# Optimization experiments

Hardware: AMD Instinct MI355X
Metric: run time of the kernel (lower is better)

## Reference

```python
import jax, jax.numpy as jnp
import numpy as np

N, B, C, H = 2048, 2, 1024, 16
HD = C // H


def setup_inputs() -> dict:
    key = jax.random.key(0)
    ks = jax.random.split(key, 11)
    s = 0.02
    return {
        "query": jax.random.normal(ks[0], (N, B, C), jnp.float32),
        "key": jax.random.normal(ks[1], (N, B, C), jnp.float32),
        "value": jax.random.normal(ks[2], (B, N, C), jnp.float32),
        "num_heads": H,
        "Wq": jax.random.normal(ks[3], (C, C), jnp.float32) * s,
        "bq": jnp.zeros((C,), jnp.float32),
        "Wk": jax.random.normal(ks[4], (C, HD), jnp.float32) * s,
        "bk": jnp.zeros((HD,), jnp.float32),
        "Wv": jax.random.normal(ks[5], (C, HD), jnp.float32) * s,
        "bv": jnp.zeros((HD,), jnp.float32),
        "Wp": jax.random.normal(ks[6], (C, C), jnp.float32) * s,
        "bp": jnp.zeros((C,), jnp.float32),
    }


def reference(query, key, value, num_heads, Wq, bq, Wk, bk, Wv, bv, Wp, bp):
    # query/key arrive seq-first (N,B,C); permute to batch-first as in torch code
    k_in = jnp.transpose(key, (1, 0, 2))    # (B, Nk, C)
    q_in = jnp.transpose(query, (1, 0, 2))  # (B, Nq, C)
    Bsz, Nq, Cd = q_in.shape
    hd = Cd // num_heads
    scale = hd ** -0.5

    # shared single K/V head (MQA)
    k = k_in @ Wk + bk                      # (B, Nk, hd)
    v = value @ Wv + bv                     # (B, Nk, hd)
    q = (q_in @ Wq + bq).reshape(Bsz, Nq, num_heads, hd)
    q = jnp.transpose(q, (0, 2, 1, 3)) * scale  # (B, H, Nq, hd)

    attn = jnp.einsum('bhqd,bkd->bhqk', q, k)   # (B, H, Nq, Nk)
    attn = jax.nn.softmax(attn, axis=-1)
    x = jnp.einsum('bhqk,bkd->bhqd', attn, v)   # (B, H, Nq, hd)
    x = jnp.transpose(x, (0, 2, 1, 3)).reshape(Bsz, Nq, Cd)
    x = x @ Wp + bp
    return jnp.transpose(x, (1, 0, 2))          # (Nq, B, C)
```

## Files before the change

### kernel.cpp

```cpp
#include <hip/hip_runtime.h>
#include <hip/hip_bf16.h>

#define DI __device__ __forceinline__

typedef float f32x4 __attribute__((ext_vector_type(4)));
typedef float f32x16 __attribute__((ext_vector_type(16)));
typedef short s16x8 __attribute__((ext_vector_type(8)));
typedef unsigned short u16x4 __attribute__((ext_vector_type(4)));
typedef unsigned long long u64;


DI unsigned short f2bf(float x) {
  union { float f; unsigned u; } v; v.f = x;
  unsigned r = 0x7fffu + ((v.u >> 16) & 1u);
  return (unsigned short)((v.u + r) >> 16);
}

DI unsigned cvtpk(float lo, float hi) {
  unsigned u;
  asm("v_cvt_pk_bf16_f32 %0, %1, %2" : "=v"(u) : "v"(lo), "v"(hi));
  return u;
}

DI f32x16 zero16() {
  f32x16 z;
#pragma unroll
  for (int i = 0; i < 16; ++i) z[i] = 0.f;
  return z;
}

DI float max16(const f32x16& a) {
  float m0 = fmaxf(a[0], a[1]),  m1 = fmaxf(a[2], a[3]);
  float m2 = fmaxf(a[4], a[5]),  m3 = fmaxf(a[6], a[7]);
  float m4 = fmaxf(a[8], a[9]),  m5 = fmaxf(a[10], a[11]);
  float m6 = fmaxf(a[12], a[13]), m7 = fmaxf(a[14], a[15]);
  m0 = fmaxf(m0, m1); m2 = fmaxf(m2, m3); m4 = fmaxf(m4, m5); m6 = fmaxf(m6, m7);
  return fmaxf(fmaxf(m0, m2), fmaxf(m4, m6));
}

DI float sum16(const f32x16& a) {
  float s0 = a[0] + a[1],  s1 = a[2] + a[3];
  float s2 = a[4] + a[5],  s3 = a[6] + a[7];
  float s4 = a[8] + a[9],  s5 = a[10] + a[11];
  float s6 = a[12] + a[13], s7 = a[14] + a[15];
  s0 += s1; s2 += s3; s4 += s5; s6 += s7;
  return (s0 + s2) + (s4 + s6);
}

DI void gll16(const void* g, void* l) {
  __builtin_amdgcn_global_load_lds(
      (const __attribute__((address_space(1))) void*)g,
      (__attribute__((address_space(3))) void*)l, 16, 0, 0);
}

DI f32x16 mfma32(s16x8 a, s16x8 b, f32x16 c) {
  return __builtin_amdgcn_mfma_f32_32x32x16_bf16(a, b, c, 0, 0, 0);
}

DI f32x4 mfma16(s16x8 a, s16x8 b, f32x4 c) {
  return __builtin_amdgcn_mfma_f32_16x16x32_bf16(a, b, c, 0, 0, 0);
}

__global__ __launch_bounds__(256) void wconv_kernel(
    const float* __restrict__ Wq, const float* __restrict__ Wk,
    const float* __restrict__ Wv, const float* __restrict__ Wp,
    unsigned short* __restrict__ WqT, unsigned short* __restrict__ WkT,
    unsigned short* __restrict__ WvT, unsigned short* __restrict__ WpT)
{
  int bid = blockIdx.x;
  const float* W; unsigned short* WT; int Ncols; int base;
  if (bid < 512)       { W = Wq; WT = WqT; Ncols = 1024; base = bid; }
  else if (bid < 1024) { W = Wp; WT = WpT; Ncols = 1024; base = bid - 512; }
  else if (bid < 1056) { W = Wk; WT = WkT; Ncols = 64;   base = bid - 1024; }
  else                 { W = Wv; WT = WvT; Ncols = 64;   base = bid - 1056; }
  int nb = base >> 5, kb = base & 31;
  int n = nb * 64 + (threadIdx.x & 63);
  int k = kb * 32 + (threadIdx.x >> 6) * 8;
  float f[8];
#pragma unroll
  for (int i = 0; i < 8; ++i) f[i] = W[(size_t)(k + i) * Ncols + n];
  union { unsigned u[4]; s16x8 v; } x;
#pragma unroll
  for (int i = 0; i < 4; ++i) x.u[i] = cvtpk(f[2 * i], f[2 * i + 1]);
  *(s16x8*)(WT + (size_t)n * 1024 + k) = x.v;
}

__global__ __launch_bounds__(256) void cvt1_kernel(
    const float* __restrict__ q, unsigned short* __restrict__ qbf)
{
  int gid = blockIdx.x * 256 + threadIdx.x;
  int row = gid >> 7;
  int c8 = (gid & 127) << 3;
  int b = row >> 11, n = row & 2047;
  size_t soff = ((size_t)n * 2 + b) * 1024 + c8;
  f32x4 v0 = *(const f32x4*)(q + soff);
  f32x4 v1 = *(const f32x4*)(q + soff + 4);
  union { unsigned u[4]; s16x8 v; } x;
  x.u[0] = cvtpk(v0.x, v0.y); x.u[1] = cvtpk(v0.z, v0.w);
  x.u[2] = cvtpk(v1.x, v1.y); x.u[3] = cvtpk(v1.z, v1.w);
  *(s16x8*)(qbf + (size_t)row * 1024 + c8) = x.v;
}

template<int MODE>
__global__ __launch_bounds__(256) void gemm16_kernel(
    const unsigned short* __restrict__ A, const unsigned short* __restrict__ Bt,
    const float* __restrict__ bias, void* __restrict__ Cpv, float scale)
{
  __shared__ __align__(16) unsigned short Asub[2][128 * 64];
  __shared__ __align__(16) unsigned short Bsub[2][64 * 64];

  const int tid = threadIdx.x;
  const int lane = tid & 63, wave = tid >> 6;
  const int l16 = lane & 15, kq = lane >> 4;
  const int wr = wave >> 1, wc = wave & 1;
  const int row0 = blockIdx.x * 128;
  const int col0 = blockIdx.y * 64;

  f32x4 acc[4][2];
#pragma unroll
  for (int mi = 0; mi < 4; ++mi)
#pragma unroll
    for (int nj = 0; nj < 2; ++nj) acc[mi][nj] = f32x4{0.f, 0.f, 0.f, 0.f};

  auto STAGE = [&](int bf, int kt) {
    const int k0 = kt * 64;
#pragma unroll
    for (int i = 0; i < 4; ++i) {
      int o = i * 4096 + tid * 16;
      int r = o >> 7, c = (o & 127) >> 1;
      gll16(A + (size_t)(row0 + r) * 1024 + k0 + c,
            (char*)Asub[bf] + i * 4096 + wave * 1024);
    }
#pragma unroll
    for (int i = 0; i < 2; ++i) {
      int o = i * 4096 + tid * 16;
      int r = o >> 7, c = (o & 127) >> 1;
      gll16(Bt + (size_t)(col0 + r) * 1024 + k0 + c,
            (char*)Bsub[bf] + i * 4096 + wave * 1024);
    }
  };

  STAGE(0, 0);
  __syncthreads();
  int cur = 0;
  for (int kt = 0; kt < 16; ++kt) {
    if (kt + 1 < 16) STAGE(cur ^ 1, kt + 1);
#pragma unroll
    for (int ks = 0; ks < 2; ++ks) {
      s16x8 af[4]; s16x8 bf2[2];
#pragma unroll
      for (int mi = 0; mi < 4; ++mi)
        af[mi] = *(const s16x8*)(Asub[cur] + (wr * 64 + mi * 16 + l16) * 64 + ks * 32 + kq * 8);
#pragma unroll
      for (int nj = 0; nj < 2; ++nj)
        bf2[nj] = *(const s16x8*)(Bsub[cur] + (wc * 32 + nj * 16 + l16) * 64 + ks * 32 + kq * 8);
#pragma unroll
      for (int mi = 0; mi < 4; ++mi)
#pragma unroll
        for (int nj = 0; nj < 2; ++nj)
          acc[mi][nj] = mfma16(af[mi], bf2[nj], acc[mi][nj]);
    }
    __syncthreads();
    cur ^= 1;
  }

#pragma unroll
  for (int mi = 0; mi < 4; ++mi)
#pragma unroll
  for (int nj = 0; nj < 2; ++nj) {
    int col = col0 + wc * 32 + nj * 16 + l16;
    int rowb = row0 + wr * 64 + mi * 16 + kq * 4;
    float bv = bias[col];
#pragma unroll
    for (int r = 0; r < 4; ++r) {
      int row = rowb + r;
      float val = acc[mi][nj][r] + bv;
      if constexpr (MODE == 0) {
        ((unsigned short*)Cpv)[(size_t)row * 1024 + col] = f2bf(val * scale);
      } else {
        ((float*)Cpv)[(size_t)(row & 2047) * 2048 + (size_t)(row >> 11) * 1024 + col] = val;
      }
    }
  }
}

__global__ __launch_bounds__(256) void gemmkv_kernel(
    const float* __restrict__ Akey, const float* __restrict__ Aval,
    const unsigned short* __restrict__ Wk, const unsigned short* __restrict__ Wv,
    float* __restrict__ part)
{
  __shared__ __align__(16) unsigned short Asub[2][64 * 64];
  __shared__ __align__(16) unsigned short Bsub[2][64 * 64];

  const int tid = threadIdx.x;
  const int lane = tid & 63, wave = tid >> 6;
  const int l16 = lane & 15, kq = lane >> 4;
  const int wr = wave >> 1, wc = wave & 1;
  const int sel = blockIdx.y;
  const float* Af = sel ? Aval : Akey;
  const unsigned short* Bt = sel ? Wv : Wk;
  const int row0 = blockIdx.x * 64;
  const int kt0 = blockIdx.z * 4, kt1 = kt0 + 4;

  const int ar = tid >> 2, ac = (tid & 3) * 16;
  const int gm = row0 + ar;
  const size_t grow = sel ? (size_t)gm * 1024
                          : (size_t)((gm & 2047) * 2 + (gm >> 11)) * 1024;

  auto LOADA = [&](int kt, f32x4* a4) {
#pragma unroll
    for (int i = 0; i < 4; ++i)
      a4[i] = *(const f32x4*)(Af + grow + kt * 64 + ac + i * 4);
  };
  auto WRITEA = [&](int bf, const f32x4* a4) {
    union { unsigned u[8]; s16x8 v[2]; } x;
#pragma unroll
    for (int i = 0; i < 4; ++i) {
      x.u[2 * i]     = cvtpk(a4[i].x, a4[i].y);
      x.u[2 * i + 1] = cvtpk(a4[i].z, a4[i].w);
    }
    *(s16x8*)(Asub[bf] + ar * 64 + ac)     = x.v[0];
    *(s16x8*)(Asub[bf] + ar * 64 + ac + 8) = x.v[1];
  };
  auto STAGEB = [&](int bf, int kt) {
#pragma unroll
    for (int i = 0; i < 2; ++i) {
      int o = i * 4096 + tid * 16;
      int r = o >> 7, c = (o & 127) >> 1;
      gll16(Bt + (size_t)r * 1024 + kt * 64 + c,
            (char*)Bsub[bf] + i * 4096 + wave * 1024);
    }
  };

  f32x4 acc[2][2];
#pragma unroll
  for (int mi = 0; mi < 2; ++mi)
#pragma unroll
    for (int nj = 0; nj < 2; ++nj) acc[mi][nj] = f32x4{0.f, 0.f, 0.f, 0.f};

  f32x4 a4[4];
  LOADA(kt0, a4);
  STAGEB(0, kt0);
  WRITEA(0, a4);
  __syncthreads();
  int cur = 0;
  for (int kt = kt0; kt < kt1; ++kt) {
    if (kt + 1 < kt1) { LOADA(kt + 1, a4); STAGEB(cur ^ 1, kt + 1); }
#pragma unroll
    for (int ks = 0; ks < 2; ++ks) {
      s16x8 af[2]; s16x8 bf2[2];
#pragma unroll
      for (int mi = 0; mi < 2; ++mi)
        af[mi] = *(const s16x8*)(Asub[cur] + (wr * 32 + mi * 16 + l16) * 64 + ks * 32 + kq * 8);
#pragma unroll
      for (int nj = 0; nj < 2; ++nj)
        bf2[nj] = *(const s16x8*)(Bsub[cur] + (wc * 32 + nj * 16 + l16) * 64 + ks * 32 + kq * 8);
#pragma unroll
      for (int mi = 0; mi < 2; ++mi)
#pragma unroll
        for (int nj = 0; nj < 2; ++nj)
          acc[mi][nj] = mfma16(af[mi], bf2[nj], acc[mi][nj]);
    }
    if (kt + 1 < kt1) WRITEA(cur ^ 1, a4);
    __syncthreads();
    cur ^= 1;
  }

#pragma unroll
  for (int mi = 0; mi < 2; ++mi)
#pragma unroll
  for (int nj = 0; nj < 2; ++nj) {
    int col = wc * 32 + nj * 16 + l16;
    int rowb = row0 + wr * 32 + mi * 16 + kq * 4;
#pragma unroll
    for (int r = 0; r < 4; ++r)
      part[(((size_t)blockIdx.z * 2 + sel) * 4096 + rowb + r) * 64 + col] = acc[mi][nj][r];
  }
}

__global__ __launch_bounds__(256) void kvreduce_kernel(
    const float* __restrict__ part, const float* __restrict__ bk,
    const float* __restrict__ bv, unsigned short* __restrict__ kproj,
    unsigned short* __restrict__ vprojT)
{
  int gid = blockIdx.x * 256 + threadIdx.x;
  int kv = gid >> 18;
  int rem = gid & 262143;
  int row = rem >> 6, col = rem & 63;
  float s = 0.f;
#pragma unroll
  for (int z = 0; z < 4; ++z)
    s += part[(((size_t)z * 2 + kv) * 4096 + row) * 64 + col];
  s += (kv ? bv : bk)[col];
  if (kv == 0)
    kproj[(size_t)row * 64 + col] = f2bf(s);
  else
    vprojT[(size_t)(row >> 11) * 131072 + (size_t)col * 2048 + (row & 2047)] = f2bf(s);
}

__global__ __launch_bounds__(512, 4) void attn_kernel(
    const unsigned short* __restrict__ qp, const unsigned short* __restrict__ kp,
    const unsigned short* __restrict__ vpt, unsigned short* __restrict__ xout)
{
  constexpr int KSTR = 72;
  __shared__ unsigned short SM[36864];
#define KBUF(c, hh) (SM + ((c) * 2 + (hh)) * (64 * KSTR))
#define VBUF(c, hh) (SM + 18432 + ((c) * 2 + (hh)) * (64 * KSTR))

  const int tid = threadIdx.x;
  const int lane = tid & 63, wave = tid >> 6;
  const int lq = lane & 31, hi = lane >> 5;
  const int qsub = wave & 3, half = wave >> 2;
  const int b = blockIdx.y >> 4, h = blockIdx.y & 15;
  const int q0 = blockIdx.x * 128 + qsub * 32;
  const size_t qrow = (size_t)(b * 2048 + q0 + lq);

  s16x8 qf[4];
#pragma unroll
  for (int s = 0; s < 4; ++s)
    qf[s] = *(const s16x8*)(qp + qrow * 1024 + h * 64 + s * 16 + hi * 8);

  f32x16 xacc0 = zero16(), xacc1 = zero16();
  float mrun = -1e30f, ssum = 0.f;

  const unsigned short* kb = kp + (size_t)b * (2048 * 64);
  const unsigned short* vb = vpt + (size_t)b * (64 * 2048);

  const int srow = tid >> 3;
  const int scol = (tid & 7) * 8;

  s16x8 kA, kB, vA, vB;
  {
    kA = *(const s16x8*)(kb + (size_t)srow * 64 + scol);
    kB = *(const s16x8*)(kb + (size_t)(16 * 64 + srow) * 64 + scol);
    vA = *(const s16x8*)(vb + (size_t)srow * 2048 + scol);
    vB = *(const s16x8*)(vb + (size_t)srow * 2048 + 16 * 64 + scol);
    *(s16x8*)(KBUF(0, 0) + srow * KSTR + scol) = kA;
    *(s16x8*)(KBUF(0, 1) + srow * KSTR + scol) = kB;
    *(s16x8*)(VBUF(0, 0) + srow * KSTR + scol) = vA;
    *(s16x8*)(VBUF(0, 1) + srow * KSTR + scol) = vB;
  }
  int cur = 0;

  for (int it = 0; it < 16; ++it) {
    __syncthreads();
    if (it + 1 < 16) {
      kA = *(const s16x8*)(kb + (size_t)((it + 1) * 64 + srow) * 64 + scol);
      kB = *(const s16x8*)(kb + (size_t)((it + 17) * 64 + srow) * 64 + scol);
      vA = *(const s16x8*)(vb + (size_t)srow * 2048 + (it + 1) * 64 + scol);
      vB = *(const s16x8*)(vb + (size_t)srow * 2048 + (it + 17) * 64 + scol);
    }
    const unsigned short* Kc = KBUF(cur, half);
    const unsigned short* Vc = VBUF(cur, half);

    f32x16 sacc0 = zero16(), sacc1 = zero16();
    __builtin_amdgcn_s_setprio(1);
#pragma unroll
    for (int s = 0; s < 4; ++s) {
      int c = s * 16 + hi * 8;
      s16x8 kf0 = *(const s16x8*)(Kc + lq * KSTR + c);
      s16x8 kf1 = *(const s16x8*)(Kc + (32 + lq) * KSTR + c);
      sacc0 = mfma32(kf0, qf[s], sacc0);
      sacc1 = mfma32(kf1, qf[s], sacc1);
    }
    __builtin_amdgcn_s_setprio(0);

    float tm = fmaxf(max16(sacc0), max16(sacc1));
    tm = fmaxf(tm, __shfl_xor(tm, 32));
    if (!__all(tm <= mrun + 8.f)) {
      float mnew = fmaxf(mrun, tm);
      float alpha = __builtin_amdgcn_exp2f(mrun - mnew);
      ssum *= alpha;
#pragma unroll
      for (int e = 0; e < 16; ++e) { xacc0[e] *= alpha; xacc1[e] *= alpha; }
      mrun = mnew;
    }
    f32x16 p0, p1;
#pragma unroll
    for (int e = 0; e < 16; ++e) p0[e] = __builtin_amdgcn_exp2f(sacc0[e] - mrun);
#pragma unroll
    for (int e = 0; e < 16; ++e) p1[e] = __builtin_amdgcn_exp2f(sacc1[e] - mrun);
    float tsum = sum16(p0) + sum16(p1);
    tsum += __shfl_xor(tsum, 32);
    ssum += tsum;

    s16x8 pb[4];
#pragma unroll
    for (int grp = 0; grp < 4; ++grp) {
      const f32x16& pp = (grp < 2) ? p0 : p1;
      const int eb = (grp & 1) * 8;
      unsigned A  = cvtpk(pp[eb + 0], pp[eb + 1]);
      unsigned Bw = cvtpk(pp[eb + 2], pp[eb + 3]);
      unsigned Cw = cvtpk(pp[eb + 4], pp[eb + 5]);
      unsigned Dw = cvtpk(pp[eb + 6], pp[eb + 7]);
      unsigned rA = (unsigned)__shfl_xor((int)(hi ? A : Cw), 32);
      unsigned rB = (unsigned)__shfl_xor((int)(hi ? Bw : Dw), 32);
      union { unsigned u[4]; s16x8 v; } pk_;
      pk_.u[0] = hi ? rA : A;
      pk_.u[1] = hi ? rB : Bw;
      pk_.u[2] = hi ? Cw : rA;
      pk_.u[3] = hi ? Dw : rB;
      pb[grp] = pk_.v;
    }

    __builtin_amdgcn_s_setprio(1);
#pragma unroll
    for (int kvs = 0; kvs < 4; ++kvs) {
      int c = kvs * 16 + hi * 8;
      s16x8 vf0 = *(const s16x8*)(Vc + lq * KSTR + c);
      s16x8 vf1 = *(const s16x8*)(Vc + (32 + lq) * KSTR + c);
      xacc0 = mfma32(vf0, pb[kvs], xacc0);
      xacc1 = mfma32(vf1, pb[kvs], xacc1);
    }
    __builtin_amdgcn_s_setprio(0);

    if (it + 1 < 16) {
      *(s16x8*)(KBUF(cur ^ 1, 0) + srow * KSTR + scol) = kA;
      *(s16x8*)(KBUF(cur ^ 1, 1) + srow * KSTR + scol) = kB;
      *(s16x8*)(VBUF(cur ^ 1, 0) + srow * KSTR + scol) = vA;
      *(s16x8*)(VBUF(cur ^ 1, 1) + srow * KSTR + scol) = vB;
      cur ^= 1;
    }
  }

  __syncthreads();
  float* msc = (float*)SM;
  const int mi_ = (qsub * 64 + lane) * 37;
  if (half == 1) {
#pragma unroll
    for (int e = 0; e < 16; ++e) { msc[mi_ + e] = xacc0[e]; msc[mi_ + 16 + e] = xacc1[e]; }
    msc[mi_ + 32] = mrun;
    msc[mi_ + 33] = ssum;
  }
  __syncthreads();
  if (half == 0) {
    float pm = msc[mi_ + 32], ps = msc[mi_ + 33];
    float mf = fmaxf(mrun, pm);
    float aa = __builtin_amdgcn_exp2f(mrun - mf);
    float bb = __builtin_amdgcn_exp2f(pm - mf);
    float inv = 1.0f / (ssum * aa + ps * bb);
#pragma unroll
    for (int dj = 0; dj < 2; ++dj) {
      const f32x16 xa = dj ? xacc1 : xacc0;
#pragma unroll
      for (int g = 0; g < 4; ++g) {
        u16x4 o4;
#pragma unroll
        for (int r = 0; r < 4; ++r) {
          int e = g * 4 + r;
          float merged = xa[e] * aa + msc[mi_ + dj * 16 + e] * bb;
          o4[r] = f2bf(merged * inv);
        }
        int d0 = dj * 32 + 8 * g + 4 * hi;
        *(u16x4*)(xout + qrow * 1024 + h * 64 + d0) = o4;
      }
    }
  }
#undef KBUF
#undef VBUF
}

extern "C" void kernel_launch(void* const* d_in, const int* in_sizes, int n_in,
                              void* d_out, int out_size, void* d_ws, size_t ws_size,
                              hipStream_t stream)
{
  const float* query = (const float*)d_in[0];
  const float* key   = (const float*)d_in[1];
  const float* value = (const float*)d_in[2];
  const float* Wq = (const float*)d_in[4];
  const float* bq = (const float*)d_in[5];
  const float* Wk = (const float*)d_in[6];
  const float* bk = (const float*)d_in[7];
  const float* Wv = (const float*)d_in[8];
  const float* bv = (const float*)d_in[9];
  const float* Wp = (const float*)d_in[10];
  const float* bp = (const float*)d_in[11];

  char* ws = (char*)d_ws;
  unsigned short* WqT    = (unsigned short*)(ws);
  unsigned short* WpT    = (unsigned short*)(ws + (2u << 20));
  unsigned short* WkT    = (unsigned short*)(ws + (4u << 20));
  unsigned short* WvT    = (unsigned short*)(ws + (4u << 20) + (128u << 10));
  unsigned short* kproj  = (unsigned short*)(ws + (5u << 20));
  unsigned short* vprojT = (unsigned short*)(ws + (5u << 20) + (512u << 10));
  unsigned short* qproj  = (unsigned short*)(ws + (6u << 20));
  unsigned short* xbuf   = (unsigned short*)(ws + (15u << 20));
  float*          part   = (float*)xbuf;
  unsigned short* qbf    = (unsigned short*)d_out;

  wconv_kernel<<<dim3(1088), 256, 0, stream>>>(Wq, Wk, Wv, Wp, WqT, WkT, WvT, WpT);
  cvt1_kernel<<<dim3(2048), 256, 0, stream>>>(query, qbf);

  const float qscale = 0.18033688011112042f;
  gemm16_kernel<0><<<dim3(32, 16), 256, 0, stream>>>(qbf, WqT, bq, qproj, qscale);
  gemmkv_kernel<<<dim3(64, 2, 4), 256, 0, stream>>>(key, value, WkT, WvT, part);
  kvreduce_kernel<<<dim3(2048), 256, 0, stream>>>(part, bk, bv, kproj, vprojT);
  attn_kernel<<<dim3(16, 32), 512, 0, stream>>>(qproj, kproj, vprojT, xbuf);
  gemm16_kernel<2><<<dim3(32, 16), 256, 0, stream>>>(xbuf, WpT, bp, d_out, 1.0f);
}
```

Baseline: 121.9 us.

## Fuse prep and projection GEMM launches, compute softmax rowsum via MFMA

Merges the weight-transpose and query-convert kernels into one prep launch, and runs the Q projection GEMM and the K/V projection GEMM in one launch using shared LDS. In attention, the softmax row sum is accumulated with an extra MFMA against a ones vector instead of VALU reductions and a shuffle, and the row max uses v_max3. The aim is to cut launch overhead and tail idle time and to shift VALU work onto the matrix cores. The cost is extra MFMA work per tile and a larger LDS footprint for the KV blocks.

```diff
diff --git a/kernel.cpp b/kernel.cpp
--- a/kernel.cpp
+++ b/kernel.cpp
@@ -22,6 +22,12 @@
   return u;
 }
 
+DI float max3f(float a, float b, float c) {
+  float d;
+  asm("v_max3_f32 %0, %1, %2, %3" : "=v"(d) : "v"(a), "v"(b), "v"(c));
+  return d;
+}
+
 DI f32x16 zero16() {
   f32x16 z;
 #pragma unroll
@@ -29,22 +35,15 @@
   return z;
 }
 
-DI float max16(const f32x16& a) {
-  float m0 = fmaxf(a[0], a[1]),  m1 = fmaxf(a[2], a[3]);
-  float m2 = fmaxf(a[4], a[5]),  m3 = fmaxf(a[6], a[7]);
-  float m4 = fmaxf(a[8], a[9]),  m5 = fmaxf(a[10], a[11]);
-  float m6 = fmaxf(a[12], a[13]), m7 = fmaxf(a[14], a[15]);
-  m0 = fmaxf(m0, m1); m2 = fmaxf(m2, m3); m4 = fmaxf(m4, m5); m6 = fmaxf(m6, m7);
-  return fmaxf(fmaxf(m0, m2), fmaxf(m4, m6));
-}
-
-DI float sum16(const f32x16& a) {
-  float s0 = a[0] + a[1],  s1 = a[2] + a[3];
-  float s2 = a[4] + a[5],  s3 = a[6] + a[7];
-  float s4 = a[8] + a[9],  s5 = a[10] + a[11];
-  float s6 = a[12] + a[13], s7 = a[14] + a[15];
-  s0 += s1; s2 += s3; s4 += s5; s6 += s7;
-  return (s0 + s2) + (s4 + s6);
+DI float max16_3(const f32x16& a) {
+  float m0 = max3f(a[0], a[1], a[2]);
+  float m1 = max3f(a[3], a[4], a[5]);
+  float m2 = max3f(a[6], a[7], a[8]);
+  float m3 = max3f(a[9], a[10], a[11]);
+  float m4 = max3f(a[12], a[13], a[14]);
+  float n0 = max3f(m0, m1, m2);
+  float n1 = max3f(m3, m4, a[15]);
+  return fmaxf(n0, n1);
 }
 
 DI void gll16(const void* g, void* l) {
@@ -61,18 +60,34 @@
   return __builtin_amdgcn_mfma_f32_16x16x32_bf16(a, b, c, 0, 0, 0);
 }
 
-__global__ __launch_bounds__(256) void wconv_kernel(
+__global__ __launch_bounds__(256) void prep_kernel(
+    const float* __restrict__ q, unsigned short* __restrict__ qbf,
     const float* __restrict__ Wq, const float* __restrict__ Wk,
     const float* __restrict__ Wv, const float* __restrict__ Wp,
     unsigned short* __restrict__ WqT, unsigned short* __restrict__ WkT,
     unsigned short* __restrict__ WvT, unsigned short* __restrict__ WpT)
 {
   int bid = blockIdx.x;
+  if (bid < 2048) {
+    int gid = bid * 256 + threadIdx.x;
+    int row = gid >> 7;
+    int c8 = (gid & 127) << 3;
+    int b = row >> 11, n = row & 2047;
+    size_t soff = ((size_t)n * 2 + b) * 1024 + c8;
+    f32x4 v0 = *(const f32x4*)(q + soff);
+    f32x4 v1 = *(const f32x4*)(q + soff + 4);
+    union { unsigned u[4]; s16x8 v; } x;
+    x.u[0] = cvtpk(v0.x, v0.y); x.u[1] = cvtpk(v0.z, v0.w);
+    x.u[2] = cvtpk(v1.x, v1.y); x.u[3] = cvtpk(v1.z, v1.w);
+    *(s16x8*)(qbf + (size_t)row * 1024 + c8) = x.v;
+    return;
+  }
+  int wb = bid - 2048;
   const float* W; unsigned short* WT; int Ncols; int base;
-  if (bid < 512)       { W = Wq; WT = WqT; Ncols = 1024; base = bid; }
-  else if (bid < 1024) { W = Wp; WT = WpT; Ncols = 1024; base = bid - 512; }
-  else if (bid < 1056) { W = Wk; WT = WkT; Ncols = 64;   base = bid - 1024; }
-  else                 { W = Wv; WT = WvT; Ncols = 64;   base = bid - 1056; }
+  if (wb < 512)       { W = Wq; WT = WqT; Ncols = 1024; base = wb; }
+  else if (wb < 1024) { W = Wp; WT = WpT; Ncols = 1024; base = wb - 512; }
+  else if (wb < 1056) { W = Wk; WT = WkT; Ncols = 64;   base = wb - 1024; }
+  else                { W = Wv; WT = WvT; Ncols = 64;   base = wb - 1056; }
   int nb = base >> 5, kb = base & 31;
   int n = nb * 64 + (threadIdx.x & 63);
   int k = kb * 32 + (threadIdx.x >> 6) * 8;
@@ -85,36 +100,19 @@
   *(s16x8*)(WT + (size_t)n * 1024 + k) = x.v;
 }
 
-__global__ __launch_bounds__(256) void cvt1_kernel(
-    const float* __restrict__ q, unsigned short* __restrict__ qbf)
-{
-  int gid = blockIdx.x * 256 + threadIdx.x;
-  int row = gid >> 7;
-  int c8 = (gid & 127) << 3;
-  int b = row >> 11, n = row & 2047;
-  size_t soff = ((size_t)n * 2 + b) * 1024 + c8;
-  f32x4 v0 = *(const f32x4*)(q + soff);
-  f32x4 v1 = *(const f32x4*)(q + soff + 4);
-  union { unsigned u[4]; s16x8 v; } x;
-  x.u[0] = cvtpk(v0.x, v0.y); x.u[1] = cvtpk(v0.z, v0.w);
-  x.u[2] = cvtpk(v1.x, v1.y); x.u[3] = cvtpk(v1.z, v1.w);
-  *(s16x8*)(qbf + (size_t)row * 1024 + c8) = x.v;
-}
-
 template<int MODE>
-__global__ __launch_bounds__(256) void gemm16_kernel(
-    const unsigned short* __restrict__ A, const unsigned short* __restrict__ Bt,
-    const float* __restrict__ bias, void* __restrict__ Cpv, float scale)
-{
-  __shared__ __align__(16) unsigned short Asub[2][128 * 64];
-  __shared__ __align__(16) unsigned short Bsub[2][64 * 64];
-
+DI void gemm16_body(const unsigned short* __restrict__ A,
+                    const unsigned short* __restrict__ Bt,
+                    const float* __restrict__ bias, void* __restrict__ Cpv,
+                    float scale, int bx, int by,
+                    unsigned short* As, unsigned short* Bs)
+{
   const int tid = threadIdx.x;
   const int lane = tid & 63, wave = tid >> 6;
   const int l16 = lane & 15, kq = lane >> 4;
   const int wr = wave >> 1, wc = wave & 1;
-  const int row0 = blockIdx.x * 128;
-  const int col0 = blockIdx.y * 64;
+  const int row0 = bx * 128;
+  const int col0 = by * 64;
 
   f32x4 acc[4][2];
 #pragma unroll
@@ -124,19 +122,19 @@
 
   auto STAGE = [&](int bf, int kt) {
     const int k0 = kt * 64;
+    char* Ad = (char*)As + bf * 16384;
+    char* Bd = (char*)Bs + bf * 8192;
 #pragma unroll
     for (int i = 0; i < 4; ++i) {
       int o = i * 4096 + tid * 16;
       int r = o >> 7, c = (o & 127) >> 1;
-      gll16(A + (size_t)(row0 + r) * 1024 + k0 + c,
-            (char*)Asub[bf] + i * 4096 + wave * 1024);
+      gll16(A + (size_t)(row0 + r) * 1024 + k0 + c, Ad + i * 4096 + wave * 1024);
     }
 #pragma unroll
     for (int i = 0; i < 2; ++i) {
       int o = i * 4096 + tid * 16;
       int r = o >> 7, c = (o & 127) >> 1;
-      gll16(Bt + (size_t)(col0 + r) * 1024 + k0 + c,
-            (char*)Bsub[bf] + i * 4096 + wave * 1024);
+      gll16(Bt + (size_t)(col0 + r) * 1024 + k0 + c, Bd + i * 4096 + wave * 1024);
     }
   };
 
@@ -150,10 +148,10 @@
       s16x8 af[4]; s16x8 bf2[2];
 #pragma unroll
       for (int mi = 0; mi < 4; ++mi)
-        af[mi] = *(const s16x8*)(Asub[cur] + (wr * 64 + mi * 16 + l16) * 64 + ks * 32 + kq * 8);
+        af[mi] = *(const s16x8*)(As + cur * 8192 + (wr * 64 + mi * 16 + l16) * 64 + ks * 32 + kq * 8);
 #pragma unroll
       for (int nj = 0; nj < 2; ++nj)
-        bf2[nj] = *(const s16x8*)(Bsub[cur] + (wc * 32 + nj * 16 + l16) * 64 + ks * 32 + kq * 8);
+        bf2[nj] = *(const s16x8*)(Bs + cur * 4096 + (wc * 32 + nj * 16 + l16) * 64 + ks * 32 + kq * 8);
 #pragma unroll
       for (int mi = 0; mi < 4; ++mi)
 #pragma unroll
@@ -184,23 +182,20 @@
   }
 }
 
-__global__ __launch_bounds__(256) void gemmkv_kernel(
-    const float* __restrict__ Akey, const float* __restrict__ Aval,
-    const unsigned short* __restrict__ Wk, const unsigned short* __restrict__ Wv,
-    float* __restrict__ part)
-{
-  __shared__ __align__(16) unsigned short Asub[2][64 * 64];
-  __shared__ __align__(16) unsigned short Bsub[2][64 * 64];
-
+DI void gemmkv_body(const float* __restrict__ Akey, const float* __restrict__ Aval,
+                    const unsigned short* __restrict__ Wk,
+                    const unsigned short* __restrict__ Wv,
+                    float* __restrict__ part, int bx, int sel, int bz,
+                    unsigned short* As, unsigned short* Bs)
+{
   const int tid = threadIdx.x;
   const int lane = tid & 63, wave = tid >> 6;
   const int l16 = lane & 15, kq = lane >> 4;
   const int wr = wave >> 1, wc = wave & 1;
-  const int sel = blockIdx.y;
   const float* Af = sel ? Aval : Akey;
   const unsigned short* Bt = sel ? Wv : Wk;
-  const int row0 = blockIdx.x * 64;
-  const int kt0 = blockIdx.z * 4, kt1 = kt0 + 4;
+  const int row0 = bx * 64;
+  const int kt0 = bz * 4, kt1 = kt0 + 4;
 
   const int ar = tid >> 2, ac = (tid & 3) * 16;
   const int gm = row0 + ar;
@@ -219,8 +214,8 @@
       x.u[2 * i]     = cvtpk(a4[i].x, a4[i].y);
       x.u[2 * i + 1] = cvtpk(a4[i].z, a4[i].w);
     }
-    *(s16x8*)(Asub[bf] + ar * 64 + ac)     = x.v[0];
-    *(s16x8*)(Asub[bf] + ar * 64 + ac + 8) = x.v[1];
+    *(s16x8*)(As + bf * 4096 + ar * 64 + ac)     = x.v[0];
+    *(s16x8*)(As + bf * 4096 + ar * 64 + ac + 8) = x.v[1];
   };
   auto STAGEB = [&](int bf, int kt) {
 #pragma unroll
@@ -228,7 +223,7 @@
       int o = i * 4096 + tid * 16;
       int r = o >> 7, c = (o & 127) >> 1;
       gll16(Bt + (size_t)r * 1024 + kt * 64 + c,
-            (char*)Bsub[bf] + i * 4096 + wave * 1024);
+            (char*)Bs + bf * 8192 + i * 4096 + wave * 1024);
     }
   };
 
@@ -251,10 +246,10 @@
       s16x8 af[2]; s16x8 bf2[2];
 #pragma unroll
       for (int mi = 0; mi < 2; ++mi)
-        af[mi] = *(const s16x8*)(Asub[cur] + (wr * 32 + mi * 16 + l16) * 64 + ks * 32 + kq * 8);
+        af[mi] = *(const s16x8*)(As + cur * 4096 + (wr * 32 + mi * 16 + l16) * 64 + ks * 32 + kq * 8);
 #pragma unroll
       for (int nj = 0; nj < 2; ++nj)
-        bf2[nj] = *(const s16x8*)(Bsub[cur] + (wc * 32 + nj * 16 + l16) * 64 + ks * 32 + kq * 8);
+        bf2[nj] = *(const s16x8*)(Bs + cur * 4096 + (wc * 32 + nj * 16 + l16) * 64 + ks * 32 + kq * 8);
 #pragma unroll
       for (int mi = 0; mi < 2; ++mi)
 #pragma unroll
@@ -274,8 +269,36 @@
     int rowb = row0 + wr * 32 + mi * 16 + kq * 4;
 #pragma unroll
     for (int r = 0; r < 4; ++r)
-      part[(((size_t)blockIdx.z * 2 + sel) * 4096 + rowb + r) * 64 + col] = acc[mi][nj][r];
-  }
+      part[(((size_t)bz * 2 + sel) * 4096 + rowb + r) * 64 + col] = acc[mi][nj][r];
+  }
+}
+
+__global__ __launch_bounds__(256) void gemmqkv_kernel(
+    const unsigned short* __restrict__ qbf, const unsigned short* __restrict__ WqT,
+    const float* __restrict__ bq, unsigned short* __restrict__ qproj, float qscale,
+    const float* __restrict__ key, const float* __restrict__ value,
+    const unsigned short* __restrict__ WkT, const unsigned short* __restrict__ WvT,
+    float* __restrict__ part)
+{
+  __shared__ __align__(16) unsigned short SMEM[24576];
+  int bid = blockIdx.x;
+  if (bid < 512) {
+    gemm16_body<0>(qbf, WqT, bq, qproj, qscale, bid & 31, bid >> 5,
+                   SMEM, SMEM + 16384);
+  } else {
+    int idx = bid - 512;
+    gemmkv_body(key, value, WkT, WvT, part, idx & 63, (idx >> 6) & 1, idx >> 7,
+                SMEM, SMEM + 8192);
+  }
+}
+
+__global__ __launch_bounds__(256) void gemmout_kernel(
+    const unsigned short* __restrict__ A, const unsigned short* __restrict__ Bt,
+    const float* __restrict__ bias, float* __restrict__ Cpv)
+{
+  __shared__ __align__(16) unsigned short SMEM[24576];
+  gemm16_body<2>(A, Bt, bias, (void*)Cpv, 1.0f, blockIdx.x, blockIdx.y,
+                 SMEM, SMEM + 16384);
 }
 
 __global__ __launch_bounds__(256) void kvreduce_kernel(
@@ -320,8 +343,12 @@
   for (int s = 0; s < 4; ++s)
     qf[s] = *(const s16x8*)(qp + qrow * 1024 + h * 64 + s * 16 + hi * 8);
 
-  f32x16 xacc0 = zero16(), xacc1 = zero16();
-  float mrun = -1e30f, ssum = 0.f;
+  s16x8 ones8;
+#pragma unroll
+  for (int i = 0; i < 8; ++i) ones8[i] = (short)0x3F80;
+
+  f32x16 xacc0 = zero16(), xacc1 = zero16(), xsum = zero16();
+  float mrun = -1e30f;
 
   const unsigned short* kb = kp + (size_t)b * (2048 * 64);
   const unsigned short* vb = vpt + (size_t)b * (64 * 2048);
@@ -365,12 +392,12 @@
     }
     __builtin_amdgcn_s_setprio(0);
 
-    float tm = fmaxf(max16(sacc0), max16(sacc1));
+    float tm = fmaxf(max16_3(sacc0), max16_3(sacc1));
     tm = fmaxf(tm, __shfl_xor(tm, 32));
     if (!__all(tm <= mrun + 8.f)) {
       float mnew = fmaxf(mrun, tm);
       float alpha = __builtin_amdgcn_exp2f(mrun - mnew);
-      ssum *= alpha;
+      xsum[0] *= alpha;
 #pragma unroll
       for (int e = 0; e < 16; ++e) { xacc0[e] *= alpha; xacc1[e] *= alpha; }
       mrun = mnew;
@@ -380,9 +407,6 @@
     for (int e = 0; e < 16; ++e) p0[e] = __builtin_amdgcn_exp2f(sacc0[e] - mrun);
 #pragma unroll
     for (int e = 0; e < 16; ++e) p1[e] = __builtin_amdgcn_exp2f(sacc1[e] - mrun);
-    float tsum = sum16(p0) + sum16(p1);
-    tsum += __shfl_xor(tsum, 32);
-    ssum += tsum;
 
     s16x8 pb[4];
 #pragma unroll
@@ -411,6 +435,7 @@
       s16x8 vf1 = *(const s16x8*)(Vc + (32 + lq) * KSTR + c);
       xacc0 = mfma32(vf0, pb[kvs], xacc0);
       xacc1 = mfma32(vf1, pb[kvs], xacc1);
+      xsum  = mfma32(ones8, pb[kvs], xsum);
     }
     __builtin_amdgcn_s_setprio(0);
 
@@ -422,6 +447,7 @@
       cur ^= 1;
     }
   }
+  const float ssum = xsum[0];
 
   __syncthreads();
   float* msc = (float*)SM;
@@ -488,13 +514,13 @@
   float*          part   = (float*)xbuf;
   unsigned short* qbf    = (unsigned short*)d_out;
 
-  wconv_kernel<<<dim3(1088), 256, 0, stream>>>(Wq, Wk, Wv, Wp, WqT, WkT, WvT, WpT);
-  cvt1_kernel<<<dim3(2048), 256, 0, stream>>>(query, qbf);
+  prep_kernel<<<dim3(3136), 256, 0, stream>>>(
+      query, qbf, Wq, Wk, Wv, Wp, WqT, WkT, WvT, WpT);
 
   const float qscale = 0.18033688011112042f;
-  gemm16_kernel<0><<<dim3(32, 16), 256, 0, stream>>>(qbf, WqT, bq, qproj, qscale);
-  gemmkv_kernel<<<dim3(64, 2, 4), 256, 0, stream>>>(key, value, WkT, WvT, part);
+  gemmqkv_kernel<<<dim3(1024), 256, 0, stream>>>(
+      qbf, WqT, bq, qproj, qscale, key, value, WkT, WvT, part);
   kvreduce_kernel<<<dim3(2048), 256, 0, stream>>>(part, bk, bv, kproj, vprojT);
   attn_kernel<<<dim3(16, 32), 512, 0, stream>>>(qproj, kproj, vprojT, xbuf);
-  gemm16_kernel<2><<<dim3(32, 16), 256, 0, stream>>>(xbuf, WpT, bp, d_out, 1.0f);
-}
+  gemmout_kernel<<<dim3(32, 16), 256, 0, stream>>>(xbuf, WpT, bp, (float*)d_out);
+}
```

Result: faster. 114.3 us (-6.2%).
